# Performance work log

Measured on AMD Instinct MI355X. Metric: run time of the kernel, lower is better.

## Reference

```python
import jax, jax.numpy as jnp
import numpy as np

N_NODES = 50000
N_EDGES = 800000
B = 512
DIM_IN = 128
D2 = 200
D3 = 200
GC1 = 100
DG = 20
DH = 64
H1 = 128
H2 = 32
BN_EPS = 1e-5


def _lin_init(k, fan_in, fan_out):
    s = 1.0 / np.sqrt(fan_in)
    kw, kb = jax.random.split(k)
    W = jax.random.uniform(kw, (fan_in, fan_out), jnp.float32, -s, s)
    b = jax.random.uniform(kb, (fan_out,), jnp.float32, -s, s)
    return W, b


def setup_inputs() -> dict:
    key = jax.random.key(0)
    ks = jax.random.split(key, 16)
    feat = jax.random.normal(ks[0], (N_NODES, DIM_IN), jnp.float32)
    desc_2d = jax.random.normal(ks[1], (B, D2), jnp.float32)
    desc_3d = jax.random.normal(ks[2], (B, D3), jnp.float32)
    src = jax.random.randint(ks[3], (N_EDGES,), 0, N_NODES, jnp.int32)
    dst = jax.random.randint(ks[4], (N_EDGES,), 0, N_NODES, jnp.int32)
    graph_id = jnp.sort(jax.random.randint(ks[5], (N_NODES,), 0, B, jnp.int32))
    gc1_W, gc1_b = _lin_init(ks[6], DIM_IN, GC1)
    gc2_W, gc2_b = _lin_init(ks[7], GC1, DG)
    pg_W, pg_b = _lin_init(ks[8], DG, DH)
    p2_W, p2_b = _lin_init(ks[9], D2, DH)
    # xavier_uniform for W2
    lim = np.sqrt(6.0 / (DH + DH))
    W2 = jax.random.uniform(ks[10], (DH, DH), jnp.float32, -lim, lim)
    fusion_dim = (DG + 1) * (D2 + 1)
    fc1_W, fc1_b = _lin_init(ks[11], fusion_dim, H1)
    fc2_W, fc2_b = _lin_init(ks[12], H1, H2)
    fc3_W, fc3_b = _lin_init(ks[13], H2, 1)
    return {
        'feat': feat, 'desc_2d': desc_2d, 'desc_3d': desc_3d,
        'gc1_W': gc1_W, 'gc1_b': gc1_b, 'gc2_W': gc2_W, 'gc2_b': gc2_b,
        'pg_W': pg_W, 'pg_b': pg_b, 'p2_W': p2_W, 'p2_b': p2_b, 'W2': W2,
        'fc1_W': fc1_W, 'fc1_b': fc1_b, 'fc2_W': fc2_W, 'fc2_b': fc2_b,
        'fc3_W': fc3_W, 'fc3_b': fc3_b,
        'bn1_g': jnp.ones((H1,), jnp.float32), 'bn1_b': jnp.zeros((H1,), jnp.float32),
        'bn2_g': jnp.ones((H2,), jnp.float32), 'bn2_b': jnp.zeros((H2,), jnp.float32),
        'src': src, 'dst': dst, 'graph_id': graph_id,
    }


def _gcn(h, src, dst, W, b):
    # copy_u -> mean over incoming mailbox -> linear apply
    agg = jax.ops.segment_sum(h[src], dst, num_segments=N_NODES)
    deg = jax.ops.segment_sum(jnp.ones((src.shape[0],), h.dtype), dst, num_segments=N_NODES)
    h_mean = agg / jnp.maximum(deg, 1.0)[:, None]  # zero in-degree -> 0 (DGL default)
    return h_mean @ W + b


def _bn(x, g, b):
    mu = x.mean(0)
    var = x.var(0)
    return (x - mu) * jax.lax.rsqrt(var + BN_EPS) * g + b


def reference(feat, desc_2d, desc_3d, gc1_W, gc1_b, gc2_W, gc2_b,
              pg_W, pg_b, p2_W, p2_b, W2,
              fc1_W, fc1_b, fc2_W, fc2_b, fc3_W, fc3_b,
              bn1_g, bn1_b, bn2_g, bn2_b, src, dst, graph_id):
    h = jax.nn.relu(_gcn(feat, src, dst, gc1_W, gc1_b))          # [N, 100]
    h = jax.nn.relu(_gcn(h, src, dst, gc2_W, gc2_b))             # [N, 20]
    # dgl.mean_nodes: per-graph mean of node features
    cnt = jax.ops.segment_sum(jnp.ones((N_NODES,), h.dtype), graph_id, num_segments=B)
    hg = jax.ops.segment_sum(h, graph_id, num_segments=B) / jnp.maximum(cnt, 1.0)[:, None]  # [B, 20]
    h_g = hg @ pg_W + pg_b                                        # [B, 64]
    h_d = desc_2d @ p2_W + p2_b                                   # [B, 64]
    s = ((h_g @ W2) * h_d).sum(-1)                                # [B]
    a = jax.nn.sigmoid(s)[:, None]                                # [B, 1]
    ones = jnp.ones((B, 1), hg.dtype)
    hg1 = jnp.concatenate([hg, ones], axis=1)                     # [B, 21]
    d1 = jnp.concatenate([a * desc_2d, ones], axis=1)             # [B, 201]
    fusion = (hg1[:, :, None] * d1[:, None, :]).reshape(B, -1)    # [B, 21*201]
    out = jax.nn.relu(_bn(fusion @ fc1_W + fc1_b, bn1_g, bn1_b))
    out = jax.nn.relu(_bn(out @ fc2_W + fc2_b, bn2_g, bn2_b))
    return out @ fc3_W + fc3_b                                    # [B, 1]
```

## Files before the change

kernel.cpp:

```cpp
#include <hip/hip_runtime.h>

#define NN 50000
#define NE 800000
#define NB 512
#define DIN 128
#define DD2 200
#define C1 100
#define C2 20
#define DHH 64
#define HH1 128
#define HH2 32
#define KD 201
#define KDP 204
#define NU 2688
#define SCB 196
#define NCT 7
#define NTILE 3125
#define GB1 782
#define FPB 3125
#define FCB 672
#define PS1 128
#define SLOT 32
#define OVFCAP 8192
#define CSTR 16

typedef short sh8 __attribute__((ext_vector_type(8)));
typedef float f32x4 __attribute__((ext_vector_type(4)));

__device__ __forceinline__ unsigned short f2bf(float x) {
    unsigned u = __float_as_uint(x);
    unsigned r = (u + 0x7fffu + ((u >> 16) & 1u)) >> 16;
    return (unsigned short)r;
}
__device__ __forceinline__ float bf_lo(unsigned u) { return __uint_as_float(u << 16); }
__device__ __forceinline__ float bf_hi(unsigned u) { return __uint_as_float(u & 0xffff0000u); }

__global__ void k_packB_init(const float* __restrict__ W, unsigned short* __restrict__ Bf,
                             int* __restrict__ cnt, float* __restrict__ hgs,
                             int* __restrict__ ovfc) {
    int idx = blockIdx.x * 256 + threadIdx.x;
    if (idx < NCT * 4 * 64) {
        int lane = idx & 63;
        int kc = (idx >> 6) & 3;
        int ct = idx >> 8;
        int col = ct * 16 + (lane & 15);
        int k0 = kc * 32 + (lane >> 4) * 8;
        unsigned short* outp = Bf + (size_t)idx * 8;
        #pragma unroll
        for (int e = 0; e < 8; ++e) {
            float v = (col < C1) ? W[(k0 + e) * C1 + col] : 0.f;
            outp[e] = f2bf(v);
        }
    }
    for (int i = idx; i < NN * CSTR; i += SCB * 256) cnt[i] = 0;
    if (idx < NB * C2) hgs[idx] = 0.f;
    if (idx == 0) *ovfc = 0;
}

__global__ __launch_bounds__(256) void k_front(const float* __restrict__ feat,
                                               const unsigned short* __restrict__ Bf,
                                               unsigned char* __restrict__ t1f8,
                                               const int* __restrict__ src,
                                               const int* __restrict__ dst,
                                               int* __restrict__ cnt,
                                               unsigned short* __restrict__ epad,
                                               int2* __restrict__ ovf,
                                               int* __restrict__ ovfc,
                                               const float* __restrict__ desc2d,
                                               const float* __restrict__ W1,
                                               float* __restrict__ V) {
    __shared__ float smem[7168];
    const int tid = threadIdx.x;

    if (blockIdx.x >= GB1 + FCB) {
        int e = (blockIdx.x - GB1 - FCB) * 256 + tid;
        if (e < NE) {
            int d = dst[e], s = src[e];
            int slot = atomicAdd(&cnt[d * CSTR], 1);
            if (slot < SLOT) {
                epad[(size_t)d * SLOT + slot] = (unsigned short)s;
            } else {
                int o = atomicAdd(ovfc, 1);
                if (o < OVFCAP) ovf[o] = make_int2(d, s);
            }
        }
        return;
    }

    if (blockIdx.x < GB1) {
        sh8* sB = (sh8*)smem;
        {
            const uint4* srcp = (const uint4*)Bf;
            uint4* dstp = (uint4*)smem;
            for (int i = tid; i < NCT * 4 * 64; i += 256) dstp[i] = srcp[i];
        }
        __syncthreads();
        const int w = tid >> 6, lane = tid & 63;
        const int ri = lane & 15;
        const int kg = lane >> 4;
        int tile = blockIdx.x * 4 + w;
        if (tile < NTILE) {
            const int n = tile * 16 + ri;
            f32x4 acc[NCT];
            #pragma unroll
            for (int ct = 0; ct < NCT; ++ct) acc[ct] = (f32x4){0.f, 0.f, 0.f, 0.f};
            #pragma unroll
            for (int kc = 0; kc < 4; ++kc) {
                const float* ap = feat + (size_t)n * DIN + kc * 32 + kg * 8;
                float4 a0 = *(const float4*)ap;
                float4 a1 = *(const float4*)(ap + 4);
                union { sh8 v; unsigned short u[8]; } af;
                af.u[0] = f2bf(a0.x); af.u[1] = f2bf(a0.y);
                af.u[2] = f2bf(a0.z); af.u[3] = f2bf(a0.w);
                af.u[4] = f2bf(a1.x); af.u[5] = f2bf(a1.y);
                af.u[6] = f2bf(a1.z); af.u[7] = f2bf(a1.w);
                #pragma unroll
                for (int ct = 0; ct < NCT; ++ct)
                    acc[ct] = __builtin_amdgcn_mfma_f32_16x16x32_bf16(
                        af.v, sB[(ct * 4 + kc) * 64 + lane], acc[ct], 0, 0, 0);
            }
            const int rbase = tile * 16 + kg * 4;
            #pragma unroll
            for (int ct = 0; ct < NCT; ++ct) {
                int col = ct * 16 + ri;
                if (col < C1) {
                    #pragma unroll
                    for (int r = 0; r < 4; ++r) {
                        int pk = __builtin_amdgcn_cvt_pk_fp8_f32(acc[ct][r], acc[ct][r], 0, false);
                        t1f8[(size_t)(rbase + r) * PS1 + col] = (unsigned char)(pk & 0xFF);
                    }
                }
            }
        }
        return;
    }

    {
        float (*S)[KDP] = (float(*)[KDP])smem;
        int fid = blockIdx.x - GB1;
        const int i = fid / 32;
        const int rem = fid % 32;
        const int bt = rem >> 1;
        const int half = rem & 1;
        for (int idx = tid; idx < 32 * 50; idx += 256) {
            int r = idx / 50, c4 = idx % 50;
            *(float4*)&S[r][c4 * 4] =
                *(const float4*)(desc2d + (size_t)(bt * 32 + r) * DD2 + c4 * 4);
        }
        __syncthreads();
        const int c = tid & 31;
        const int rg = tid >> 5;
        float acc[4][2];
        #pragma unroll
        for (int r = 0; r < 4; ++r) { acc[r][0] = 0.f; acc[r][1] = 0.f; }
        const float* Wb = W1 + (size_t)i * (KD * HH1) + half * 64 + c;
        for (int k = 0; k < 200; k += 4) {
            const float* Wk = Wb + (size_t)k * HH1;
            float w0[2], w1[2], w2[2], w3[2];
            #pragma unroll
            for (int m = 0; m < 2; ++m) {
                w0[m] = Wk[32 * m];
                w1[m] = Wk[HH1 + 32 * m];
                w2[m] = Wk[2 * HH1 + 32 * m];
                w3[m] = Wk[3 * HH1 + 32 * m];
            }
            #pragma unroll
            for (int r = 0; r < 4; ++r) {
                float4 a4 = *(const float4*)&S[rg * 4 + r][k];
                #pragma unroll
                for (int m = 0; m < 2; ++m)
                    acc[r][m] += a4.x * w0[m] + a4.y * w1[m] + a4.z * w2[m] + a4.w * w3[m];
            }
        }
        #pragma unroll
        for (int r = 0; r < 4; ++r) {
            int b = bt * 32 + rg * 4 + r;
            float* Vr = V + (size_t)b * NU + i * HH1 + half * 64 + c;
            Vr[0] = acc[r][0];
            Vr[32] = acc[r][1];
        }
    }
}

__global__ __launch_bounds__(1024) void k_agg1g2(const unsigned char* __restrict__ t1f8,
                                                 const int* __restrict__ cnt,
                                                 const unsigned short* __restrict__ epad,
                                                 const int2* __restrict__ ovf,
                                                 const int* __restrict__ ovfc,
                                                 const float* __restrict__ b1,
                                                 const float* __restrict__ W2,
                                                 unsigned* __restrict__ t2b) {
    __shared__ float sW2[C1 * C2];
    __shared__ float sh1[16][C1];
    __shared__ float sc[16][C2];
    const int tid = threadIdx.x;
    for (int idx = tid; idx < C1 * C2; idx += 1024) sW2[idx] = W2[idx];
    const int w = tid >> 6, l = tid & 63;
    const int n = blockIdx.x * 16 + w;
    if (l < 50) {
        const int deg = cnt[n * CSTR];
        const int m = deg < SLOT ? deg : SLOT;
        const unsigned short* ep = epad + (size_t)n * SLOT;
        const int co = 2 * l;
        float acc0 = 0.f, acc1 = 0.f;
        int e = 0;
        for (; e + 7 < m; e += 8) {
            int s0 = ep[e],     s1 = ep[e + 1], s2 = ep[e + 2], s3 = ep[e + 3];
            int s4 = ep[e + 4], s5 = ep[e + 5], s6 = ep[e + 6], s7 = ep[e + 7];
            int u0 = *(const unsigned short*)(t1f8 + (size_t)s0 * PS1 + co);
            int u1 = *(const unsigned short*)(t1f8 + (size_t)s1 * PS1 + co);
            int u2 = *(const unsigned short*)(t1f8 + (size_t)s2 * PS1 + co);
            int u3 = *(const unsigned short*)(t1f8 + (size_t)s3 * PS1 + co);
            int u4 = *(const unsigned short*)(t1f8 + (size_t)s4 * PS1 + co);
            int u5 = *(const unsigned short*)(t1f8 + (size_t)s5 * PS1 + co);
            int u6 = *(const unsigned short*)(t1f8 + (size_t)s6 * PS1 + co);
            int u7 = *(const unsigned short*)(t1f8 + (size_t)s7 * PS1 + co);
            acc0 += __builtin_amdgcn_cvt_f32_fp8(u0, 0); acc1 += __builtin_amdgcn_cvt_f32_fp8(u0, 1);
            acc0 += __builtin_amdgcn_cvt_f32_fp8(u1, 0); acc1 += __builtin_amdgcn_cvt_f32_fp8(u1, 1);
            acc0 += __builtin_amdgcn_cvt_f32_fp8(u2, 0); acc1 += __builtin_amdgcn_cvt_f32_fp8(u2, 1);
            acc0 += __builtin_amdgcn_cvt_f32_fp8(u3, 0); acc1 += __builtin_amdgcn_cvt_f32_fp8(u3, 1);
            acc0 += __builtin_amdgcn_cvt_f32_fp8(u4, 0); acc1 += __builtin_amdgcn_cvt_f32_fp8(u4, 1);
            acc0 += __builtin_amdgcn_cvt_f32_fp8(u5, 0); acc1 += __builtin_amdgcn_cvt_f32_fp8(u5, 1);
            acc0 += __builtin_amdgcn_cvt_f32_fp8(u6, 0); acc1 += __builtin_amdgcn_cvt_f32_fp8(u6, 1);
            acc0 += __builtin_amdgcn_cvt_f32_fp8(u7, 0); acc1 += __builtin_amdgcn_cvt_f32_fp8(u7, 1);
        }
        for (; e < m; ++e) {
            int u = *(const unsigned short*)(t1f8 + (size_t)ep[e] * PS1 + co);
            acc0 += __builtin_amdgcn_cvt_f32_fp8(u, 0);
            acc1 += __builtin_amdgcn_cvt_f32_fp8(u, 1);
        }
        if (deg > SLOT) {
            int novf = *ovfc; novf = novf < OVFCAP ? novf : OVFCAP;
            for (int j2 = 0; j2 < novf; ++j2) {
                int2 p = ovf[j2];
                if (p.x == n) {
                    int u = *(const unsigned short*)(t1f8 + (size_t)p.y * PS1 + co);
                    acc0 += __builtin_amdgcn_cvt_f32_fp8(u, 0);
                    acc1 += __builtin_amdgcn_cvt_f32_fp8(u, 1);
                }
            }
        }
        float d = (float)(deg > 0 ? deg : 1);
        sh1[w][2 * l]     = fmaxf(acc0 / d + b1[2 * l], 0.f);
        sh1[w][2 * l + 1] = fmaxf(acc1 / d + b1[2 * l + 1], 0.f);
    }
    __syncthreads();
    if (tid < 16 * C2) {
        int ln = tid / C2, j = tid % C2;
        float acc = 0.f;
        #pragma unroll 4
        for (int k = 0; k < C1; ++k) acc += sh1[ln][k] * sW2[k * C2 + j];
        sc[ln][j] = acc;
    }
    __syncthreads();
    if (tid < 16 * 10) {
        int r = tid / 10, jp = tid % 10;
        t2b[(size_t)(blockIdx.x * 16 + r) * 10 + jp] =
            (unsigned)f2bf(sc[r][2 * jp]) | ((unsigned)f2bf(sc[r][2 * jp + 1]) << 16);
    }
}

__global__ void k_agg2p(const unsigned* __restrict__ t2b, const int* __restrict__ cnt,
                        const unsigned short* __restrict__ epad, const int2* __restrict__ ovf,
                        const int* __restrict__ ovfc, const float* __restrict__ bias,
                        const int* __restrict__ gid, float* __restrict__ hgs) {
    int ln = threadIdx.x / C2, c = threadIdx.x % C2;
    if (ln >= 12) return;
    int n = blockIdx.x * 12 + ln;
    if (n >= NN) return;
    const int deg = cnt[n * CSTR];
    const int m = deg < SLOT ? deg : SLOT;
    const unsigned short* ep = epad + (size_t)n * SLOT;
    const int jp = c >> 1, hi = c & 1;
    float acc = 0.f;
    int e = 0;
    for (; e + 3 < m; e += 4) {
        int s0 = ep[e], s1 = ep[e + 1], s2 = ep[e + 2], s3 = ep[e + 3];
        unsigned u0 = t2b[(size_t)s0 * 10 + jp];
        unsigned u1 = t2b[(size_t)s1 * 10 + jp];
        unsigned u2 = t2b[(size_t)s2 * 10 + jp];
        unsigned u3 = t2b[(size_t)s3 * 10 + jp];
        acc += hi ? bf_hi(u0) : bf_lo(u0);
        acc += hi ? bf_hi(u1) : bf_lo(u1);
        acc += hi ? bf_hi(u2) : bf_lo(u2);
        acc += hi ? bf_hi(u3) : bf_lo(u3);
    }
    for (; e < m; ++e) {
        unsigned u = t2b[(size_t)ep[e] * 10 + jp];
        acc += hi ? bf_hi(u) : bf_lo(u);
    }
    if (deg > SLOT) {
        int novf = *ovfc; novf = novf < OVFCAP ? novf : OVFCAP;
        for (int j2 = 0; j2 < novf; ++j2) {
            int2 p = ovf[j2];
            if (p.x == n) {
                unsigned u = t2b[(size_t)p.y * 10 + jp];
                acc += hi ? bf_hi(u) : bf_lo(u);
            }
        }
    }
    float d = (float)(deg > 0 ? deg : 1);
    float v = acc / d + bias[c];
    v = v > 0.f ? v : 0.f;
    atomicAdd(&hgs[gid[n] * C2 + c], v);
}

__global__ __launch_bounds__(128) void k_hfc1(const float* __restrict__ hgs,
                                              const int* __restrict__ gid,
                                              const float* __restrict__ desc2d,
                                              const float* __restrict__ pgW,
                                              const float* __restrict__ pgb,
                                              const float* __restrict__ p2W,
                                              const float* __restrict__ p2b,
                                              const float* __restrict__ W2,
                                              const float* __restrict__ V,
                                              const float* __restrict__ W1,
                                              float* __restrict__ o1) {
    __shared__ float shg[C2];
    __shared__ float sg[DHH];
    __shared__ float sa;
    const int b = blockIdx.x, tid = threadIdx.x;
    if (tid < C2) {
        int lo = 0, hi = NN;
        while (lo < hi) { int m = (lo + hi) >> 1; if (gid[m] < b) lo = m + 1; else hi = m; }
        int lo2 = lo, hi2 = NN;
        while (lo2 < hi2) { int m = (lo2 + hi2) >> 1; if (gid[m] < b + 1) lo2 = m + 1; else hi2 = m; }
        float dcnt = (float)(lo2 - lo);
        if (dcnt < 1.f) dcnt = 1.f;
        shg[tid] = hgs[b * C2 + tid] / dcnt;
    }
    __syncthreads();
    float hdj = 0.f;
    if (tid < DHH) {
        float hgj = pgb[tid];
        #pragma unroll
        for (int k = 0; k < C2; ++k) hgj += shg[k] * pgW[k * DHH + tid];
        hdj = p2b[tid];
        #pragma unroll 4
        for (int k = 0; k < DD2; ++k) hdj += desc2d[b * DD2 + k] * p2W[k * DHH + tid];
        sg[tid] = hgj;
    }
    __syncthreads();
    if (tid < DHH) {
        float tj = 0.f;
        #pragma unroll 4
        for (int k = 0; k < DHH; ++k) tj += sg[k] * W2[k * DHH + tid];
        float v = tj * hdj;
        #pragma unroll
        for (int off = 32; off; off >>= 1) v += __shfl_xor(v, off, 64);
        if (tid == 0) sa = 1.f / (1.f + expf(-v));
    }
    __syncthreads();
    const int j = tid;
    const float* Vb = V + (size_t)b * NU + j;
    const float* WL = W1 + (size_t)200 * HH1 + j;
    float sv = Vb[20 * HH1];
    float sw = WL[(size_t)20 * KD * HH1];
    #pragma unroll
    for (int i = 0; i < 20; ++i) {
        float h = shg[i];
        sv += h * Vb[i * HH1];
        sw += h * WL[(size_t)i * KD * HH1];
    }
    o1[b * HH1 + j] = sa * sv + sw;
}

__global__ __launch_bounds__(128) void k_fc2s(const float* __restrict__ o1,
                                              const float* __restrict__ g,
                                              const float* __restrict__ beta,
                                              const float* __restrict__ W,
                                              float* __restrict__ o2) {
    __shared__ float r[HH1];
    __shared__ float part[4][HH2];
    const int tid = threadIdx.x;
    float s = 0.f, s2 = 0.f;
    for (int b = 0; b < NB; ++b) {
        float v = o1[b * HH1 + tid];
        s += v; s2 += v * v;
    }
    float mu = s / NB;
    float rstd = rsqrtf(s2 / NB - mu * mu + 1e-5f);
    float scale = rstd * g[tid];
    float shift = beta[tid] - mu * scale;
    const int m = tid & 31, p = tid >> 5;
    for (int q = 0; q < 4; ++q) {
        int b = blockIdx.x * 4 + q;
        float v = o1[b * HH1 + tid];
        __syncthreads();
        r[tid] = fmaxf(v * scale + shift, 0.f);
        __syncthreads();
        float acc = 0.f;
        #pragma unroll 4
        for (int j = p * 32; j < p * 32 + 32; ++j) acc += r[j] * W[j * HH2 + m];
        part[p][m] = acc;
        __syncthreads();
        if (tid < HH2) o2[b * HH2 + tid] = part[0][tid] + part[1][tid] + part[2][tid] + part[3][tid];
    }
}

__global__ __launch_bounds__(512) void k_finals(const float* __restrict__ o2,
                                                const float* __restrict__ g,
                                                const float* __restrict__ beta,
                                                const float* __restrict__ W3,
                                                const float* __restrict__ b3,
                                                float* __restrict__ out) {
    __shared__ float ps[16][HH2], ps2[16][HH2];
    __shared__ float sscale[HH2], sshift[HH2];
    const int tid = threadIdx.x;
    const int gq = tid >> 5, m = tid & 31;
    float s = 0.f, s2 = 0.f;
    for (int rr = 0; rr < 32; ++rr) {
        float v = o2[(gq * 32 + rr) * HH2 + m];
        s += v; s2 += v * v;
    }
    ps[gq][m] = s; ps2[gq][m] = s2;
    __syncthreads();
    if (tid < HH2) {
        float ts = 0.f, ts2 = 0.f;
        #pragma unroll
        for (int q = 0; q < 16; ++q) { ts += ps[q][tid]; ts2 += ps2[q][tid]; }
        float mu = ts / NB;
        float rstd = rsqrtf(ts2 / NB - mu * mu + 1e-5f);
        float scale = rstd * g[tid];
        sscale[tid] = scale;
        sshift[tid] = beta[tid] - mu * scale;
    }
    __syncthreads();
    float acc = b3[0];
    #pragma unroll 4
    for (int mm = 0; mm < HH2; ++mm) {
        float v = o2[tid * HH2 + mm];
        acc += fmaxf(v * sscale[mm] + sshift[mm], 0.f) * W3[mm];
    }
    out[tid] = acc;
}

extern "C" void kernel_launch(void* const* d_in, const int* in_sizes, int n_in,
                              void* d_out, int out_size, void* d_ws, size_t ws_size,
                              hipStream_t stream) {
    const float* feat   = (const float*)d_in[0];
    const float* desc2d = (const float*)d_in[1];
    const float* gc1W = (const float*)d_in[3];
    const float* gc1b = (const float*)d_in[4];
    const float* gc2W = (const float*)d_in[5];
    const float* gc2b = (const float*)d_in[6];
    const float* pgW  = (const float*)d_in[7];
    const float* pgb  = (const float*)d_in[8];
    const float* p2W  = (const float*)d_in[9];
    const float* p2b  = (const float*)d_in[10];
    const float* W2   = (const float*)d_in[11];
    const float* fc1W = (const float*)d_in[12];
    const float* fc2W = (const float*)d_in[14];
    const float* fc3W = (const float*)d_in[16];
    const float* fc3b = (const float*)d_in[17];
    const float* bn1g = (const float*)d_in[18];
    const float* bn1b = (const float*)d_in[19];
    const float* bn2g = (const float*)d_in[20];
    const float* bn2b = (const float*)d_in[21];
    const int* src = (const int*)d_in[22];
    const int* dst = (const int*)d_in[23];
    const int* gid = (const int*)d_in[24];
    float* out = (float*)d_out;

    char* ws = (char*)d_ws;
    size_t off = 0;
    auto alloc = [&](size_t nb) {
        void* p = ws + off;
        off = (off + nb + 255) & ~(size_t)255;
        return p;
    };
    unsigned char* t1f8 = (unsigned char*)alloc((size_t)NN * PS1);
    unsigned* t2b = (unsigned*)alloc((size_t)NN * 10 * 4);
    int* cnt_in  = (int*)alloc((size_t)NN * CSTR * 4);
    unsigned short* epad = (unsigned short*)alloc((size_t)NN * SLOT * 2);
    int2* ovf    = (int2*)alloc((size_t)OVFCAP * 8);
    int* ovfc    = (int*)alloc(256);
    unsigned short* Bf = (unsigned short*)alloc((size_t)NCT * 4 * 64 * 16);
    float* V     = (float*)alloc((size_t)NB * NU * 4);
    float* hgs   = (float*)alloc((size_t)NB * C2 * 4);
    float* o1    = (float*)alloc((size_t)NB * HH1 * 4);
    float* o2    = (float*)alloc((size_t)NB * HH2 * 4);

    k_packB_init<<<SCB, 256, 0, stream>>>(gc1W, Bf, cnt_in, hgs, ovfc);
    k_front<<<GB1 + FCB + FPB, 256, 0, stream>>>(feat, Bf, t1f8, src, dst, cnt_in,
                                                 epad, ovf, ovfc, desc2d, fc1W, V);

    k_agg1g2<<<NTILE, 1024, 0, stream>>>(t1f8, cnt_in, epad, ovf, ovfc, gc1b, gc2W, t2b);
    k_agg2p<<<(NN + 11) / 12, 256, 0, stream>>>(t2b, cnt_in, epad, ovf, ovfc, gc2b, gid, hgs);

    k_hfc1<<<NB, 128, 0, stream>>>(hgs, gid, desc2d, pgW, pgb, p2W, p2b, W2, V, fc1W, o1);
    k_fc2s<<<NB / 4, 128, 0, stream>>>(o1, bn1g, bn1b, fc2W, o2);
    k_finals<<<1, 512, 0, stream>>>(o2, bn2g, bn2b, fc3W, fc3b, out);
}
```

Measured before the change: 182.6 us.

## Fuse tail kernels into one launch using last-block-done atomic counter

Merges the fc1-combine, BN1+fc2, and BN2+fc3 kernels into a single kernel. Each block computes its o1 row and then increments a global done counter, and the last block to finish runs the batch-norm statistics, fc2 and fc3 serially. This removes two kernel launches and their inter-kernel gaps. In exchange, the fc2 stage that previously ran across 128 blocks now runs in one 256-thread block, which lengthens the serial tail.

```diff
diff --git a/kernel.cpp b/kernel.cpp
--- a/kernel.cpp
+++ b/kernel.cpp
@@ -37,7 +37,7 @@
 
 __global__ void k_packB_init(const float* __restrict__ W, unsigned short* __restrict__ Bf,
                              int* __restrict__ cnt, float* __restrict__ hgs,
-                             int* __restrict__ ovfc) {
+                             int* __restrict__ ovfc, int* __restrict__ done) {
     int idx = blockIdx.x * 256 + threadIdx.x;
     if (idx < NCT * 4 * 64) {
         int lane = idx & 63;
@@ -54,7 +54,7 @@
     }
     for (int i = idx; i < NN * CSTR; i += SCB * 256) cnt[i] = 0;
     if (idx < NB * C2) hgs[idx] = 0.f;
-    if (idx == 0) *ovfc = 0;
+    if (idx == 0) { *ovfc = 0; *done = 0; }
 }
 
 __global__ __launch_bounds__(256) void k_front(const float* __restrict__ feat,
@@ -305,7 +305,7 @@
     atomicAdd(&hgs[gid[n] * C2 + c], v);
 }
 
-__global__ __launch_bounds__(128) void k_hfc1(const float* __restrict__ hgs,
+__global__ __launch_bounds__(256) void k_tail(const float* __restrict__ hgs,
                                               const int* __restrict__ gid,
                                               const float* __restrict__ desc2d,
                                               const float* __restrict__ pgW,
@@ -315,10 +315,21 @@
                                               const float* __restrict__ W2,
                                               const float* __restrict__ V,
                                               const float* __restrict__ W1,
-                                              float* __restrict__ o1) {
+                                              float* __restrict__ o1,
+                                              const float* __restrict__ fc2W,
+                                              const float* __restrict__ bn1g,
+                                              const float* __restrict__ bn1b,
+                                              float* __restrict__ o2,
+                                              const float* __restrict__ bn2g,
+                                              const float* __restrict__ bn2b,
+                                              const float* __restrict__ W3,
+                                              const float* __restrict__ b3,
+                                              float* __restrict__ out,
+                                              int* __restrict__ done) {
     __shared__ float shg[C2];
     __shared__ float sg[DHH];
     __shared__ float sa;
+    __shared__ int amLastS;
     const int b = blockIdx.x, tid = threadIdx.x;
     if (tid < C2) {
         int lo = 0, hi = NN;
@@ -351,88 +362,99 @@
         if (tid == 0) sa = 1.f / (1.f + expf(-v));
     }
     __syncthreads();
-    const int j = tid;
-    const float* Vb = V + (size_t)b * NU + j;
-    const float* WL = W1 + (size_t)200 * HH1 + j;
-    float sv = Vb[20 * HH1];
-    float sw = WL[(size_t)20 * KD * HH1];
-    #pragma unroll
-    for (int i = 0; i < 20; ++i) {
-        float h = shg[i];
-        sv += h * Vb[i * HH1];
-        sw += h * WL[(size_t)i * KD * HH1];
-    }
-    o1[b * HH1 + j] = sa * sv + sw;
-}
-
-__global__ __launch_bounds__(128) void k_fc2s(const float* __restrict__ o1,
-                                              const float* __restrict__ g,
-                                              const float* __restrict__ beta,
-                                              const float* __restrict__ W,
-                                              float* __restrict__ o2) {
-    __shared__ float r[HH1];
-    __shared__ float part[4][HH2];
-    const int tid = threadIdx.x;
-    float s = 0.f, s2 = 0.f;
-    for (int b = 0; b < NB; ++b) {
-        float v = o1[b * HH1 + tid];
-        s += v; s2 += v * v;
-    }
-    float mu = s / NB;
-    float rstd = rsqrtf(s2 / NB - mu * mu + 1e-5f);
-    float scale = rstd * g[tid];
-    float shift = beta[tid] - mu * scale;
-    const int m = tid & 31, p = tid >> 5;
-    for (int q = 0; q < 4; ++q) {
-        int b = blockIdx.x * 4 + q;
-        float v = o1[b * HH1 + tid];
-        __syncthreads();
-        r[tid] = fmaxf(v * scale + shift, 0.f);
-        __syncthreads();
-        float acc = 0.f;
+    if (tid < HH1) {
+        const int j = tid;
+        const float* Vb = V + (size_t)b * NU + j;
+        const float* WL = W1 + (size_t)200 * HH1 + j;
+        float sv = Vb[20 * HH1];
+        float sw = WL[(size_t)20 * KD * HH1];
+        #pragma unroll
+        for (int i = 0; i < 20; ++i) {
+            float h = shg[i];
+            sv += h * Vb[i * HH1];
+            sw += h * WL[(size_t)i * KD * HH1];
+        }
+        o1[b * HH1 + j] = sa * sv + sw;
+    }
+    __threadfence();
+    if (tid == 0)
+        amLastS = (__hip_atomic_fetch_add(done, 1, __ATOMIC_ACQ_REL,
+                                          __HIP_MEMORY_SCOPE_AGENT) == NB - 1);
+    __syncthreads();
+    if (!amLastS) return;
+
+    __shared__ float st1a[2][HH1], st1b[2][HH1];
+    __shared__ float sc1[HH1], sh1s[HH1];
+    __shared__ float rbuf[4][HH1];
+    __shared__ float ps[8][HH2], ps2[8][HH2];
+    __shared__ float sc2[HH2], sh2s[HH2];
+    {
+        const int j = tid & 127, h = tid >> 7;
+        float s = 0.f, s2 = 0.f;
+        for (int b2 = h * 256; b2 < h * 256 + 256; ++b2) {
+            float v = o1[b2 * HH1 + j];
+            s += v; s2 += v * v;
+        }
+        st1a[h][j] = s; st1b[h][j] = s2;
+    }
+    __syncthreads();
+    if (tid < HH1) {
+        float s = st1a[0][tid] + st1a[1][tid];
+        float s2 = st1b[0][tid] + st1b[1][tid];
+        float mu = s / NB;
+        float rstd = rsqrtf(s2 / NB - mu * mu + 1e-5f);
+        float sc = rstd * bn1g[tid];
+        sc1[tid] = sc;
+        sh1s[tid] = bn1b[tid] - mu * sc;
+    }
+    __syncthreads();
+    {
+        const int wv = tid >> 6, l = tid & 63;
+        const int m = l & 31, hh = l >> 5;
+        for (int r0 = wv; r0 < NB; r0 += 4) {
+            float v0 = o1[r0 * HH1 + l];
+            float v1 = o1[r0 * HH1 + 64 + l];
+            rbuf[wv][l] = fmaxf(v0 * sc1[l] + sh1s[l], 0.f);
+            rbuf[wv][64 + l] = fmaxf(v1 * sc1[64 + l] + sh1s[64 + l], 0.f);
+            float acc = 0.f;
+            #pragma unroll 8
+            for (int j2 = hh * 64; j2 < hh * 64 + 64; ++j2)
+                acc += rbuf[wv][j2] * fc2W[j2 * HH2 + m];
+            acc += __shfl_xor(acc, 32, 64);
+            if (l < 32) o2[r0 * HH2 + m] = acc;
+        }
+    }
+    __syncthreads();
+    {
+        const int m = tid & 31, q = tid >> 5;
+        float s = 0.f, s2 = 0.f;
+        for (int r = q * 64; r < q * 64 + 64; ++r) {
+            float v = o2[r * HH2 + m];
+            s += v; s2 += v * v;
+        }
+        ps[q][m] = s; ps2[q][m] = s2;
+    }
+    __syncthreads();
+    if (tid < HH2) {
+        float s = 0.f, s2 = 0.f;
+        #pragma unroll
+        for (int q = 0; q < 8; ++q) { s += ps[q][tid]; s2 += ps2[q][tid]; }
+        float mu = s / NB;
+        float rstd = rsqrtf(s2 / NB - mu * mu + 1e-5f);
+        float sc = rstd * bn2g[tid];
+        sc2[tid] = sc;
+        sh2s[tid] = bn2b[tid] - mu * sc;
+    }
+    __syncthreads();
+    for (int b2 = tid; b2 < NB; b2 += 256) {
+        float acc = b3[0];
         #pragma unroll 4
-        for (int j = p * 32; j < p * 32 + 32; ++j) acc += r[j] * W[j * HH2 + m];
-        part[p][m] = acc;
-        __syncthreads();
-        if (tid < HH2) o2[b * HH2 + tid] = part[0][tid] + part[1][tid] + part[2][tid] + part[3][tid];
-    }
-}
-
-__global__ __launch_bounds__(512) void k_finals(const float* __restrict__ o2,
-                                                const float* __restrict__ g,
-                                                const float* __restrict__ beta,
-                                                const float* __restrict__ W3,
-                                                const float* __restrict__ b3,
-                                                float* __restrict__ out) {
-    __shared__ float ps[16][HH2], ps2[16][HH2];
-    __shared__ float sscale[HH2], sshift[HH2];
-    const int tid = threadIdx.x;
-    const int gq = tid >> 5, m = tid & 31;
-    float s = 0.f, s2 = 0.f;
-    for (int rr = 0; rr < 32; ++rr) {
-        float v = o2[(gq * 32 + rr) * HH2 + m];
-        s += v; s2 += v * v;
-    }
-    ps[gq][m] = s; ps2[gq][m] = s2;
-    __syncthreads();
-    if (tid < HH2) {
-        float ts = 0.f, ts2 = 0.f;
-        #pragma unroll
-        for (int q = 0; q < 16; ++q) { ts += ps[q][tid]; ts2 += ps2[q][tid]; }
-        float mu = ts / NB;
-        float rstd = rsqrtf(ts2 / NB - mu * mu + 1e-5f);
-        float scale = rstd * g[tid];
-        sscale[tid] = scale;
-        sshift[tid] = beta[tid] - mu * scale;
-    }
-    __syncthreads();
-    float acc = b3[0];
-    #pragma unroll 4
-    for (int mm = 0; mm < HH2; ++mm) {
-        float v = o2[tid * HH2 + mm];
-        acc += fmaxf(v * sscale[mm] + sshift[mm], 0.f) * W3[mm];
-    }
-    out[tid] = acc;
+        for (int mm = 0; mm < HH2; ++mm) {
+            float v = o2[b2 * HH2 + mm];
+            acc += fmaxf(v * sc2[mm] + sh2s[mm], 0.f) * W3[mm];
+        }
+        out[b2] = acc;
+    }
 }
 
 extern "C" void kernel_launch(void* const* d_in, const int* in_sizes, int n_in,
@@ -475,20 +497,20 @@
     unsigned short* epad = (unsigned short*)alloc((size_t)NN * SLOT * 2);
     int2* ovf    = (int2*)alloc((size_t)OVFCAP * 8);
     int* ovfc    = (int*)alloc(256);
+    int* done    = (int*)alloc(256);
     unsigned short* Bf = (unsigned short*)alloc((size_t)NCT * 4 * 64 * 16);
     float* V     = (float*)alloc((size_t)NB * NU * 4);
     float* hgs   = (float*)alloc((size_t)NB * C2 * 4);
     float* o1    = (float*)alloc((size_t)NB * HH1 * 4);
     float* o2    = (float*)alloc((size_t)NB * HH2 * 4);
 
-    k_packB_init<<<SCB, 256, 0, stream>>>(gc1W, Bf, cnt_in, hgs, ovfc);
+    k_packB_init<<<SCB, 256, 0, stream>>>(gc1W, Bf, cnt_in, hgs, ovfc, done);
     k_front<<<GB1 + FCB + FPB, 256, 0, stream>>>(feat, Bf, t1f8, src, dst, cnt_in,
                                                  epad, ovf, ovfc, desc2d, fc1W, V);
 
     k_agg1g2<<<NTILE, 1024, 0, stream>>>(t1f8, cnt_in, epad, ovf, ovfc, gc1b, gc2W, t2b);
     k_agg2p<<<(NN + 11) / 12, 256, 0, stream>>>(t2b, cnt_in, epad, ovf, ovfc, gc2b, gid, hgs);
 
-    k_hfc1<<<NB, 128, 0, stream>>>(hgs, gid, desc2d, pgW, pgb, p2W, p2b, W2, V, fc1W, o1);
-    k_fc2s<<<NB / 4, 128, 0, stream>>>(o1, bn1g, bn1b, fc2W, o2);
-    k_finals<<<1, 512, 0, stream>>>(o2, bn2g, bn2b, fc3W, fc3b, out);
-}
+    k_tail<<<NB, 256, 0, stream>>>(hgs, gid, desc2d, pgW, pgb, p2W, p2b, W2, V, fc1W, o1,
+                                   fc2W, bn1g, bn1b, o2, bn2g, bn2b, fc3W, fc3b, out, done);
+}
```

Result: slower. 357.8 us (+96.0%).
